# Kernel tuning notes

Measured on AMD Instinct MI355X. Metric: run time of the kernel, lower is better.

## Reference

```python
import jax, jax.numpy as jnp
import numpy as np

NQ, M, ND, N, H, DIM = 32, 32, 200, 160, 768, 128
TEMP = 0.1      # log_softmax temperature
TAU = 0.5       # gumbel-softmax temperature
NEG = -10000.0


def _l2norm(x):
    # F.normalize(p=2, dim=-1) with eps clamp
    n = jnp.maximum(jnp.linalg.norm(x, axis=-1, keepdims=True), 1e-12)
    return x / n


def setup_inputs() -> dict:
    key = jax.random.key(0)
    k1, k2, k3, k4, k5, k6 = jax.random.split(key, 6)
    Q = jax.random.normal(k1, (NQ, M, H), dtype=jnp.float32)
    D = jax.random.normal(k2, (ND, N, H), dtype=jnp.float32)
    q_mask = jax.random.randint(k3, (NQ, M), 0, 2).astype(jnp.float32)
    d_mask = jax.random.randint(k4, (ND, N), 0, 2).astype(jnp.float32)
    # pre-sampled Gumbel(0,1) noise for gumbel_softmax (fixed for determinism)
    u = jax.random.uniform(k5, (NQ, ND, M, N), dtype=jnp.float32,
                           minval=1e-6, maxval=1.0 - 1e-6)
    gumbel_noise = -jnp.log(-jnp.log(u))
    # proj_linear: Linear(768, dim, bias=False)
    W_proj = jax.random.normal(k6, (H, DIM), dtype=jnp.float32) / np.sqrt(H)
    return {"Q": Q, "D": D, "q_mask": q_mask, "d_mask": d_mask,
            "gumbel_noise": gumbel_noise, "W_proj": W_proj}


def reference(Q, D, q_mask, d_mask, gumbel_noise, W_proj):
    # project + L2-normalize token embeddings
    Qp = _l2norm(Q @ W_proj)            # [q, m, dim]
    Dp = _l2norm(D @ W_proj)            # [d, n, dim]

    # pairwise token similarities: [q, d, m, n]
    sim = jnp.einsum('qmh,dnh->qdmn', Qp, Dp)

    dm = d_mask[None, :, None, :]       # [1, d, 1, n]
    sim_masked = sim * dm + (1.0 - dm) * NEG

    logits = jax.nn.log_softmax(sim_masked / TEMP, axis=-1)

    # gumbel_softmax(tau=0.5, hard=True) with straight-through
    y_soft = jax.nn.softmax((logits + gumbel_noise) / TAU, axis=-1)
    idx = jnp.argmax(y_soft, axis=-1)
    y_hard = jax.nn.one_hot(idx, N, dtype=y_soft.dtype)
    y = jax.lax.stop_gradient(y_hard - y_soft) + y_soft

    # select doc token per query token, mask query tokens, sum -> [q, d]
    scores = (y * sim_masked).sum(-1)          # [q, d, m]
    scores = scores * q_mask[:, None, :]
    return scores.sum(-1)                      # [q, d]
```

## Files before the change

### kernel.cpp

```cpp
#include <hip/hip_runtime.h>
#include <math.h>

#define NQ_   32
#define M_    32
#define ND_   200
#define N_    160
#define H_    768
#define DIM_  128
#define DROWS_ (ND_ * N_)
#define QROWS_ (NQ_ * M_)
#define TROWS_ (DROWS_ + QROWS_)

__device__ __forceinline__ void gl_lds16(const float* g, float* l) {
    __builtin_amdgcn_global_load_lds(
        (const __attribute__((address_space(1))) unsigned int*)g,
        (__attribute__((address_space(3))) unsigned int*)l, 16, 0, 0);
}

__global__ __launch_bounds__(128) void proj_kernel(
    const float* __restrict__ Dmat, const float* __restrict__ Qmat,
    const float* __restrict__ W, float* __restrict__ DpT,
    float* __restrict__ QpT)
{
    __shared__ __align__(16) float Xt[2][16][32];
    __shared__ __align__(16) float Ws[2][16][128];
    const int tid  = threadIdx.x;
    const int lane = tid & 63;
    const int wv   = tid >> 6;
    const int rb   = blockIdx.x * 32;
    const int cg   = tid & 15;
    const int rg   = tid >> 4;
    const int xrow = tid >> 2;
    const int xc4  = tid & 3;

    const int rX = rb + xrow;
    const float* xr = (rX < DROWS_) ? (Dmat + (size_t)rX * H_)
                                    : (Qmat + (size_t)(rX - DROWS_) * H_);

    float acc[4][8];
#pragma unroll
    for (int i = 0; i < 4; ++i)
#pragma unroll
        for (int j = 0; j < 8; ++j) acc[i][j] = 0.0f;

#pragma unroll
    for (int t = 0; t < 4; ++t) {
        const int part = wv * 4 + t;
        gl_lds16(W + part * 256 + lane * 4, &Ws[0][0][0] + part * 256);
    }
    float4 xreg = *reinterpret_cast<const float4*>(xr + xc4 * 4);

    for (int c = 0; c < 48; ++c) {
        const int cb = c & 1;
        Xt[cb][xc4*4+0][xrow] = xreg.x;
        Xt[cb][xc4*4+1][xrow] = xreg.y;
        Xt[cb][xc4*4+2][xrow] = xreg.z;
        Xt[cb][xc4*4+3][xrow] = xreg.w;
        __syncthreads();
        if (c < 47) {
            const int kc = (c + 1) * 16;
            const float* wsrc = W + (size_t)kc * DIM_;
            float* wdst = &Ws[cb ^ 1][0][0];
#pragma unroll
            for (int t = 0; t < 4; ++t) {
                const int part = wv * 4 + t;
                gl_lds16(wsrc + part * 256 + lane * 4, wdst + part * 256);
            }
            xreg = *reinterpret_cast<const float4*>(xr + kc + xc4 * 4);
        }
        __builtin_amdgcn_sched_barrier(0);
#pragma unroll
        for (int k = 0; k < 16; ++k) {
            float a[4], b[8];
            *reinterpret_cast<float4*>(&a[0]) = *reinterpret_cast<const float4*>(&Xt[cb][k][rg*4]);
            *reinterpret_cast<float4*>(&b[0]) = *reinterpret_cast<const float4*>(&Ws[cb][k][cg*8]);
            *reinterpret_cast<float4*>(&b[4]) = *reinterpret_cast<const float4*>(&Ws[cb][k][cg*8+4]);
#pragma unroll
            for (int i = 0; i < 4; ++i)
#pragma unroll
                for (int j = 0; j < 8; ++j)
                    acc[i][j] = fmaf(a[i], b[j], acc[i][j]);
        }
    }

    float nrm[4];
#pragma unroll
    for (int i = 0; i < 4; ++i) {
        float ss = 0.0f;
#pragma unroll
        for (int j = 0; j < 8; ++j) ss = __fadd_rn(ss, __fmul_rn(acc[i][j], acc[i][j]));
        ss = __fadd_rn(ss, __shfl_xor(ss, 1));
        ss = __fadd_rn(ss, __shfl_xor(ss, 2));
        ss = __fadd_rn(ss, __shfl_xor(ss, 4));
        ss = __fadd_rn(ss, __shfl_xor(ss, 8));
        nrm[i] = fmaxf(sqrtf(ss), 1e-12f);
    }

    if (rb < DROWS_) {
        const int dd = rb / 160, n0 = rb - dd * 160;
        float* o = DpT + (size_t)dd * (DIM_ * N_) + n0 + rg * 4;
#pragma unroll
        for (int j = 0; j < 8; ++j) {
            float4 v;
            v.x = acc[0][j] / nrm[0];
            v.y = acc[1][j] / nrm[1];
            v.z = acc[2][j] / nrm[2];
            v.w = acc[3][j] / nrm[3];
            *reinterpret_cast<float4*>(o + (size_t)(cg*8 + j) * N_) = v;
        }
    } else {
        const int rq = rb - DROWS_;
        const int qq = rq >> 5;
        float* o = QpT + (size_t)qq * (DIM_ * M_) + rg * 4;
#pragma unroll
        for (int j = 0; j < 8; ++j) {
            float4 v;
            v.x = acc[0][j] / nrm[0];
            v.y = acc[1][j] / nrm[1];
            v.z = acc[2][j] / nrm[2];
            v.w = acc[3][j] / nrm[3];
            *reinterpret_cast<float4*>(o + (size_t)(cg*8 + j) * M_) = v;
        }
    }
}

__global__ __launch_bounds__(128) void score_kernel(
    const float* __restrict__ QpT, const float* __restrict__ DpT,
    const float* __restrict__ qmask, const float* __restrict__ dmask,
    const float* __restrict__ gum, float* __restrict__ out)
{
    __shared__ __align__(16) float Qt[2][8][32];
    __shared__ __align__(16) float Dt[2][8][160];
    __shared__ float red[2];
    const int tid  = threadIdx.x;
    const int lane = tid & 63;
    const int wv   = tid >> 6;
    const int mg   = tid >> 4;
    const int ng   = tid & 15;
    const int q    = blockIdx.x & 31;
    const int d    = blockIdx.x >> 5;

    const float* Qb = QpT + (size_t)q * (DIM_ * M_);
    const float* Db = DpT + (size_t)d * (DIM_ * N_);

    float acc[4][10];
#pragma unroll
    for (int i = 0; i < 4; ++i)
#pragma unroll
        for (int j = 0; j < 10; ++j) acc[i][j] = 0.0f;

    if (wv == 0) {
        gl_lds16(Qb + lane * 4, &Qt[0][0][0]);
        gl_lds16(Db + lane * 4, &Dt[0][0][0]);
        gl_lds16(Db + 256 + lane * 4, &Dt[0][0][0] + 256);
    } else {
        gl_lds16(Db + 512  + lane * 4, &Dt[0][0][0] + 512);
        gl_lds16(Db + 768  + lane * 4, &Dt[0][0][0] + 768);
        gl_lds16(Db + 1024 + lane * 4, &Dt[0][0][0] + 1024);
    }

    for (int c = 0; c < 16; ++c) {
        const int cb = c & 1;
        __syncthreads();
        if (c < 15) {
            const float* qsrc = Qb + (size_t)(c + 1) * 8 * M_;
            const float* dsrc = Db + (size_t)(c + 1) * 8 * N_;
            float* qdst = &Qt[cb ^ 1][0][0];
            float* ddst = &Dt[cb ^ 1][0][0];
            if (wv == 0) {
                gl_lds16(qsrc + lane * 4, qdst);
                gl_lds16(dsrc + lane * 4, ddst);
                gl_lds16(dsrc + 256 + lane * 4, ddst + 256);
            } else {
                gl_lds16(dsrc + 512  + lane * 4, ddst + 512);
                gl_lds16(dsrc + 768  + lane * 4, ddst + 768);
                gl_lds16(dsrc + 1024 + lane * 4, ddst + 1024);
            }
        }
        __builtin_amdgcn_sched_barrier(0);
#pragma unroll
        for (int k = 0; k < 8; ++k) {
            float a[4], b[10];
            *reinterpret_cast<float4*>(&a[0]) = *reinterpret_cast<const float4*>(&Qt[cb][k][mg*4]);
            const float* bp = &Dt[cb][k][ng*10];
#pragma unroll
            for (int j2 = 0; j2 < 5; ++j2)
                *reinterpret_cast<float2*>(&b[j2*2]) = *reinterpret_cast<const float2*>(&bp[j2*2]);
#pragma unroll
            for (int i = 0; i < 4; ++i)
#pragma unroll
                for (int j = 0; j < 10; ++j)
                    acc[i][j] = fmaf(a[i], b[j], acc[i][j]);
        }
    }

    float dmv[10];
    {
        const float* dmp = dmask + (size_t)d * N_ + ng * 10;
#pragma unroll
        for (int j2 = 0; j2 < 5; ++j2)
            *reinterpret_cast<float2*>(&dmv[j2*2]) = *reinterpret_cast<const float2*>(&dmp[j2*2]);
    }

    const float* gq = gum + ((size_t)q * ND_ + d) * ((size_t)M_ * N_);

    float g[2][10];
    {
        const float2* gp = reinterpret_cast<const float2*>(&gq[(size_t)(mg*4) * N_ + ng*10]);
#pragma unroll
        for (int j2 = 0; j2 < 5; ++j2)
            *reinterpret_cast<float2*>(&g[0][j2*2]) = gp[j2];
    }

    float partial = 0.0f;
#pragma unroll
    for (int i = 0; i < 4; ++i) {
        const int m = mg * 4 + i;
        float x[10];
        float mx = -3.402823466e38f;
#pragma unroll
        for (int j = 0; j < 10; ++j) {
            float sm = (dmv[j] != 0.0f) ? acc[i][j] : -10000.0f;
            x[j] = sm / 0.1f;
            mx = fmaxf(mx, x[j]);
        }
        if (i < 3) {
            const float2* gp = reinterpret_cast<const float2*>(&gq[(size_t)(m + 1) * N_ + ng*10]);
#pragma unroll
            for (int j2 = 0; j2 < 5; ++j2)
                *reinterpret_cast<float2*>(&g[(i+1)&1][j2*2]) = gp[j2];
        }
        mx = fmaxf(mx, __shfl_xor(mx, 1));
        mx = fmaxf(mx, __shfl_xor(mx, 2));
        mx = fmaxf(mx, __shfl_xor(mx, 4));
        mx = fmaxf(mx, __shfl_xor(mx, 8));

        float se = 0.0f;
#pragma unroll
        for (int j = 0; j < 10; ++j) se = __fadd_rn(se, expf(x[j] - mx));
        se = __fadd_rn(se, __shfl_xor(se, 1));
        se = __fadd_rn(se, __shfl_xor(se, 2));
        se = __fadd_rn(se, __shfl_xor(se, 4));
        se = __fadd_rn(se, __shfl_xor(se, 8));
        const float lse = logf(se);

        float z[10];
        float mz = -3.402823466e38f;
#pragma unroll
        for (int j = 0; j < 10; ++j) {
            z[j] = ((x[j] - mx - lse) + g[i&1][j]) / 0.5f;
            mz = fmaxf(mz, z[j]);
        }
        mz = fmaxf(mz, __shfl_xor(mz, 1));
        mz = fmaxf(mz, __shfl_xor(mz, 2));
        mz = fmaxf(mz, __shfl_xor(mz, 4));
        mz = fmaxf(mz, __shfl_xor(mz, 8));

        float e2[10];
        float s2 = 0.0f;
#pragma unroll
        for (int j = 0; j < 10; ++j) { e2[j] = expf(z[j] - mz); s2 = __fadd_rn(s2, e2[j]); }
        s2 = __fadd_rn(s2, __shfl_xor(s2, 1));
        s2 = __fadd_rn(s2, __shfl_xor(s2, 2));
        s2 = __fadd_rn(s2, __shfl_xor(s2, 4));
        s2 = __fadd_rn(s2, __shfl_xor(s2, 8));

        float besty = -1.0f; int bestn = 0x7fffffff; float bests = 0.0f;
#pragma unroll
        for (int j = 0; j < 10; ++j) {
            float y = e2[j] / s2;
            if (y > besty) {
                besty = y;
                bestn = ng*10 + j;
                bests = (dmv[j] != 0.0f) ? acc[i][j] : -10000.0f;
            }
        }
#pragma unroll
        for (int dl = 1; dl < 16; dl <<= 1) {
            float oy = __shfl_xor(besty, dl);
            int   on = __shfl_xor(bestn, dl);
            float os = __shfl_xor(bests, dl);
            if (oy > besty || (oy == besty && on < bestn)) {
                besty = oy; bestn = on; bests = os;
            }
        }
        const float qmv = qmask[q * M_ + m];
        if (ng == 0) partial = __fadd_rn(partial, __fmul_rn(bests, qmv));
    }
    partial = __fadd_rn(partial, __shfl_xor(partial, 16));
    partial = __fadd_rn(partial, __shfl_xor(partial, 32));
    if (lane == 0) red[wv] = partial;
    __syncthreads();
    if (tid == 0) out[(size_t)q * ND_ + d] = __fadd_rn(red[0], red[1]);
}

extern "C" void kernel_launch(void* const* d_in, const int* in_sizes, int n_in,
                              void* d_out, int out_size, void* d_ws, size_t ws_size,
                              hipStream_t stream)
{
    const float* Q   = (const float*)d_in[0];
    const float* D   = (const float*)d_in[1];
    const float* qm  = (const float*)d_in[2];
    const float* dm  = (const float*)d_in[3];
    const float* gum = (const float*)d_in[4];
    const float* W   = (const float*)d_in[5];
    float* out = (float*)d_out;

    float* QpT = (float*)d_ws;
    float* DpT = QpT + (size_t)QROWS_ * DIM_;

    proj_kernel<<<dim3(TROWS_ / 32), dim3(128), 0, stream>>>(D, Q, W, DpT, QpT);
    score_kernel<<<dim3(NQ_ * ND_), dim3(128), 0, stream>>>(QpT, DpT, qm, dm, gum, out);
}
```

Baseline: 509.0 us.

## Triple-buffer projection and score loads; single-wave score blocks without barriers

The projection kernel now uses a three-slot ring buffer for W tiles and waits on explicit vmcnt counters before each barrier, so loads run two chunks ahead. The score kernel drops to one 64-thread wave per (q,d) pair, with each thread owning 8 query rows. That wave-local design lets it replace __syncthreads with vmcnt waits on a three-deep LDS pipeline and skip the final shared-memory reduction. Gumbel-noise and qmask loads are issued earlier. The cost is more registers per thread and fewer threads per block, which may lower occupancy and latency hiding, and the hand-tuned waitcnt values must match the number of loads in flight.

Result: slower. 649.3 us (+27.6%).

```diff
diff --git a/kernel.cpp b/kernel.cpp
--- a/kernel.cpp
+++ b/kernel.cpp
@@ -17,13 +17,16 @@
         (__attribute__((address_space(3))) unsigned int*)l, 16, 0, 0);
 }
 
+#define ASM_VMCNT(n) asm volatile("s_waitcnt vmcnt(" #n ")" ::: "memory")
+#define ASM_LGKM0    asm volatile("s_waitcnt lgkmcnt(0)" ::: "memory")
+
 __global__ __launch_bounds__(128) void proj_kernel(
     const float* __restrict__ Dmat, const float* __restrict__ Qmat,
     const float* __restrict__ W, float* __restrict__ DpT,
     float* __restrict__ QpT)
 {
     __shared__ __align__(16) float Xt[2][16][32];
-    __shared__ __align__(16) float Ws[2][16][128];
+    __shared__ __align__(16) float Ws[3][16][128];
     const int tid  = threadIdx.x;
     const int lane = tid & 63;
     const int wv   = tid >> 6;
@@ -34,8 +37,8 @@
     const int xc4  = tid & 3;
 
     const int rX = rb + xrow;
-    const float* xr = (rX < DROWS_) ? (Dmat + (size_t)rX * H_)
-                                    : (Qmat + (size_t)(rX - DROWS_) * H_);
+    const float* xr_ptr = (rX < DROWS_) ? (Dmat + (size_t)rX * H_)
+                                        : (Qmat + (size_t)(rX - DROWS_) * H_);
 
     float acc[4][8];
 #pragma unroll
@@ -48,38 +51,86 @@
         const int part = wv * 4 + t;
         gl_lds16(W + part * 256 + lane * 4, &Ws[0][0][0] + part * 256);
     }
-    float4 xreg = *reinterpret_cast<const float4*>(xr + xc4 * 4);
-
-    for (int c = 0; c < 48; ++c) {
-        const int cb = c & 1;
-        Xt[cb][xc4*4+0][xrow] = xreg.x;
-        Xt[cb][xc4*4+1][xrow] = xreg.y;
-        Xt[cb][xc4*4+2][xrow] = xreg.z;
-        Xt[cb][xc4*4+3][xrow] = xreg.w;
-        __syncthreads();
-        if (c < 47) {
-            const int kc = (c + 1) * 16;
-            const float* wsrc = W + (size_t)kc * DIM_;
-            float* wdst = &Ws[cb ^ 1][0][0];
-#pragma unroll
-            for (int t = 0; t < 4; ++t) {
-                const int part = wv * 4 + t;
-                gl_lds16(wsrc + part * 256 + lane * 4, wdst + part * 256);
-            }
-            xreg = *reinterpret_cast<const float4*>(xr + kc + xc4 * 4);
-        }
-        __builtin_amdgcn_sched_barrier(0);
-#pragma unroll
-        for (int k = 0; k < 16; ++k) {
-            float a[4], b[8];
-            *reinterpret_cast<float4*>(&a[0]) = *reinterpret_cast<const float4*>(&Xt[cb][k][rg*4]);
-            *reinterpret_cast<float4*>(&b[0]) = *reinterpret_cast<const float4*>(&Ws[cb][k][cg*8]);
-            *reinterpret_cast<float4*>(&b[4]) = *reinterpret_cast<const float4*>(&Ws[cb][k][cg*8+4]);
-#pragma unroll
-            for (int i = 0; i < 4; ++i)
-#pragma unroll
-                for (int j = 0; j < 8; ++j)
-                    acc[i][j] = fmaf(a[i], b[j], acc[i][j]);
+    float4 xr0 = *reinterpret_cast<const float4*>(xr_ptr + 0 + xc4 * 4);
+#pragma unroll
+    for (int t = 0; t < 4; ++t) {
+        const int part = wv * 4 + t;
+        gl_lds16(W + 16 * DIM_ + part * 256 + lane * 4, &Ws[1][0][0] + part * 256);
+    }
+    float4 xr1 = *reinterpret_cast<const float4*>(xr_ptr + 16 + xc4 * 4);
+
+    int b0 = 0;
+    for (int c = 0; c < 48; c += 2) {
+        {
+            Xt[0][xc4*4+0][xrow] = xr0.x;
+            Xt[0][xc4*4+1][xrow] = xr0.y;
+            Xt[0][xc4*4+2][xrow] = xr0.z;
+            Xt[0][xc4*4+3][xrow] = xr0.w;
+            ASM_VMCNT(5);
+            ASM_LGKM0;
+            __builtin_amdgcn_s_barrier();
+            if (c + 2 < 48) {
+                const int kc = (c + 2) * 16;
+                const int b2 = (b0 + 2 >= 3) ? b0 - 1 : b0 + 2;
+                float* wdst = &Ws[0][0][0] + b2 * 2048;
+                const float* wsrc = W + (size_t)kc * DIM_;
+#pragma unroll
+                for (int t = 0; t < 4; ++t) {
+                    const int part = wv * 4 + t;
+                    gl_lds16(wsrc + part * 256 + lane * 4, wdst + part * 256);
+                }
+                xr0 = *reinterpret_cast<const float4*>(xr_ptr + kc + xc4 * 4);
+            }
+            __builtin_amdgcn_sched_barrier(0);
+            const float* wb = &Ws[0][0][0] + b0 * 2048;
+#pragma unroll
+            for (int k = 0; k < 16; ++k) {
+                float a[4], b[8];
+                *reinterpret_cast<float4*>(&a[0]) = *reinterpret_cast<const float4*>(&Xt[0][k][rg*4]);
+                *reinterpret_cast<float4*>(&b[0]) = *reinterpret_cast<const float4*>(wb + k*128 + cg*8);
+                *reinterpret_cast<float4*>(&b[4]) = *reinterpret_cast<const float4*>(wb + k*128 + cg*8 + 4);
+#pragma unroll
+                for (int i = 0; i < 4; ++i)
+#pragma unroll
+                    for (int j = 0; j < 8; ++j)
+                        acc[i][j] = fmaf(a[i], b[j], acc[i][j]);
+            }
+        }
+        {
+            const int b1 = (b0 + 1 >= 3) ? b0 - 2 : b0 + 1;
+            Xt[1][xc4*4+0][xrow] = xr1.x;
+            Xt[1][xc4*4+1][xrow] = xr1.y;
+            Xt[1][xc4*4+2][xrow] = xr1.z;
+            Xt[1][xc4*4+3][xrow] = xr1.w;
+            ASM_VMCNT(5);
+            ASM_LGKM0;
+            __builtin_amdgcn_s_barrier();
+            if (c + 3 < 48) {
+                const int kc = (c + 3) * 16;
+                float* wdst = &Ws[0][0][0] + b0 * 2048;
+                const float* wsrc = W + (size_t)kc * DIM_;
+#pragma unroll
+                for (int t = 0; t < 4; ++t) {
+                    const int part = wv * 4 + t;
+                    gl_lds16(wsrc + part * 256 + lane * 4, wdst + part * 256);
+                }
+                xr1 = *reinterpret_cast<const float4*>(xr_ptr + kc + xc4 * 4);
+            }
+            __builtin_amdgcn_sched_barrier(0);
+            const float* wb = &Ws[0][0][0] + b1 * 2048;
+#pragma unroll
+            for (int k = 0; k < 16; ++k) {
+                float a[4], b[8];
+                *reinterpret_cast<float4*>(&a[0]) = *reinterpret_cast<const float4*>(&Xt[1][k][rg*4]);
+                *reinterpret_cast<float4*>(&b[0]) = *reinterpret_cast<const float4*>(wb + k*128 + cg*8);
+                *reinterpret_cast<float4*>(&b[4]) = *reinterpret_cast<const float4*>(wb + k*128 + cg*8 + 4);
+#pragma unroll
+                for (int i = 0; i < 4; ++i)
+#pragma unroll
+                    for (int j = 0; j < 8; ++j)
+                        acc[i][j] = fmaf(a[i], b[j], acc[i][j]);
+            }
+            b0 = (b0 + 2 >= 3) ? b0 - 1 : b0 + 2;
         }
     }
 
@@ -124,76 +175,31 @@
     }
 }
 
-__global__ __launch_bounds__(128) void score_kernel(
+__global__ __launch_bounds__(64) void score_kernel(
     const float* __restrict__ QpT, const float* __restrict__ DpT,
     const float* __restrict__ qmask, const float* __restrict__ dmask,
     const float* __restrict__ gum, float* __restrict__ out)
 {
-    __shared__ __align__(16) float Qt[2][8][32];
-    __shared__ __align__(16) float Dt[2][8][160];
-    __shared__ float red[2];
-    const int tid  = threadIdx.x;
-    const int lane = tid & 63;
-    const int wv   = tid >> 6;
-    const int mg   = tid >> 4;
-    const int ng   = tid & 15;
+    __shared__ __align__(16) float Qt[3][8][32];
+    __shared__ __align__(16) float Dt[3][8][160];
+    const int lane = threadIdx.x;
+    const int mg   = lane >> 4;
+    const int ng   = lane & 15;
     const int q    = blockIdx.x & 31;
     const int d    = blockIdx.x >> 5;
 
     const float* Qb = QpT + (size_t)q * (DIM_ * M_);
     const float* Db = DpT + (size_t)d * (DIM_ * N_);
-
-    float acc[4][10];
-#pragma unroll
-    for (int i = 0; i < 4; ++i)
-#pragma unroll
-        for (int j = 0; j < 10; ++j) acc[i][j] = 0.0f;
-
-    if (wv == 0) {
-        gl_lds16(Qb + lane * 4, &Qt[0][0][0]);
-        gl_lds16(Db + lane * 4, &Dt[0][0][0]);
-        gl_lds16(Db + 256 + lane * 4, &Dt[0][0][0] + 256);
-    } else {
-        gl_lds16(Db + 512  + lane * 4, &Dt[0][0][0] + 512);
-        gl_lds16(Db + 768  + lane * 4, &Dt[0][0][0] + 768);
-        gl_lds16(Db + 1024 + lane * 4, &Dt[0][0][0] + 1024);
-    }
-
-    for (int c = 0; c < 16; ++c) {
-        const int cb = c & 1;
-        __syncthreads();
-        if (c < 15) {
-            const float* qsrc = Qb + (size_t)(c + 1) * 8 * M_;
-            const float* dsrc = Db + (size_t)(c + 1) * 8 * N_;
-            float* qdst = &Qt[cb ^ 1][0][0];
-            float* ddst = &Dt[cb ^ 1][0][0];
-            if (wv == 0) {
-                gl_lds16(qsrc + lane * 4, qdst);
-                gl_lds16(dsrc + lane * 4, ddst);
-                gl_lds16(dsrc + 256 + lane * 4, ddst + 256);
-            } else {
-                gl_lds16(dsrc + 512  + lane * 4, ddst + 512);
-                gl_lds16(dsrc + 768  + lane * 4, ddst + 768);
-                gl_lds16(dsrc + 1024 + lane * 4, ddst + 1024);
-            }
-        }
-        __builtin_amdgcn_sched_barrier(0);
-#pragma unroll
-        for (int k = 0; k < 8; ++k) {
-            float a[4], b[10];
-            *reinterpret_cast<float4*>(&a[0]) = *reinterpret_cast<const float4*>(&Qt[cb][k][mg*4]);
-            const float* bp = &Dt[cb][k][ng*10];
-#pragma unroll
-            for (int j2 = 0; j2 < 5; ++j2)
-                *reinterpret_cast<float2*>(&b[j2*2]) = *reinterpret_cast<const float2*>(&bp[j2*2]);
-#pragma unroll
-            for (int i = 0; i < 4; ++i)
-#pragma unroll
-                for (int j = 0; j < 10; ++j)
-                    acc[i][j] = fmaf(a[i], b[j], acc[i][j]);
-        }
-    }
-
+    const float* gq = gum + ((size_t)q * ND_ + d) * ((size_t)M_ * N_);
+
+    float g[2][10];
+#pragma unroll
+    for (int r = 0; r < 2; ++r) {
+        const float2* gp = reinterpret_cast<const float2*>(&gq[(size_t)(mg*8 + r) * N_ + ng*10]);
+#pragma unroll
+        for (int j2 = 0; j2 < 5; ++j2)
+            *reinterpret_cast<float2*>(&g[r][j2*2]) = gp[j2];
+    }
     float dmv[10];
     {
         const float* dmp = dmask + (size_t)d * N_ + ng * 10;
@@ -201,21 +207,64 @@
         for (int j2 = 0; j2 < 5; ++j2)
             *reinterpret_cast<float2*>(&dmv[j2*2]) = *reinterpret_cast<const float2*>(&dmp[j2*2]);
     }
-
-    const float* gq = gum + ((size_t)q * ND_ + d) * ((size_t)M_ * N_);
-
-    float g[2][10];
-    {
-        const float2* gp = reinterpret_cast<const float2*>(&gq[(size_t)(mg*4) * N_ + ng*10]);
-#pragma unroll
-        for (int j2 = 0; j2 < 5; ++j2)
-            *reinterpret_cast<float2*>(&g[0][j2*2]) = gp[j2];
-    }
+    float qmv[8];
+#pragma unroll
+    for (int i = 0; i < 8; ++i) qmv[i] = qmask[q * M_ + mg*8 + i];
+
+    float acc[8][10];
+#pragma unroll
+    for (int i = 0; i < 8; ++i)
+#pragma unroll
+        for (int j = 0; j < 10; ++j) acc[i][j] = 0.0f;
+
+#define ISSUE_CHUNK(c_)                                                     \
+    do {                                                                    \
+        const int b_ = (c_) % 3;                                            \
+        const float* qs_ = Qb + (size_t)(c_) * 8 * M_;                      \
+        const float* ds_ = Db + (size_t)(c_) * 8 * N_;                      \
+        float* qd_ = &Qt[b_][0][0];                                         \
+        float* dd_ = &Dt[b_][0][0];                                         \
+        gl_lds16(qs_ + lane * 4, qd_);                                      \
+        gl_lds16(ds_ + 0   + lane * 4, dd_ + 0);                            \
+        gl_lds16(ds_ + 256 + lane * 4, dd_ + 256);                          \
+        gl_lds16(ds_ + 512 + lane * 4, dd_ + 512);                          \
+        gl_lds16(ds_ + 768 + lane * 4, dd_ + 768);                          \
+        gl_lds16(ds_ + 1024 + lane * 4, dd_ + 1024);                        \
+    } while (0)
+
+    ISSUE_CHUNK(0);
+    ISSUE_CHUNK(1);
+
+    for (int c = 0; c < 16; ++c) {
+        if (c < 15) { ASM_VMCNT(6); }
+        else        { ASM_VMCNT(0); }
+        if (c < 14) ISSUE_CHUNK(c + 2);
+        __builtin_amdgcn_sched_barrier(0);
+        const int cb = c % 3;
+        const float* qtb = &Qt[cb][0][0];
+        const float* dtb = &Dt[cb][0][0];
+#pragma unroll
+        for (int k = 0; k < 8; ++k) {
+            float a[8], b[10];
+            *reinterpret_cast<float4*>(&a[0]) = *reinterpret_cast<const float4*>(qtb + k*32 + mg*8);
+            *reinterpret_cast<float4*>(&a[4]) = *reinterpret_cast<const float4*>(qtb + k*32 + mg*8 + 4);
+            const float* bp = dtb + k*160 + ng*10;
+#pragma unroll
+            for (int j2 = 0; j2 < 5; ++j2)
+                *reinterpret_cast<float2*>(&b[j2*2]) = *reinterpret_cast<const float2*>(&bp[j2*2]);
+#pragma unroll
+            for (int i = 0; i < 8; ++i)
+#pragma unroll
+                for (int j = 0; j < 10; ++j)
+                    acc[i][j] = fmaf(a[i], b[j], acc[i][j]);
+        }
+    }
+#undef ISSUE_CHUNK
 
     float partial = 0.0f;
 #pragma unroll
-    for (int i = 0; i < 4; ++i) {
-        const int m = mg * 4 + i;
+    for (int i = 0; i < 8; ++i) {
+        const int m = mg*8 + i;
         float x[10];
         float mx = -3.402823466e38f;
 #pragma unroll
@@ -223,12 +272,6 @@
             float sm = (dmv[j] != 0.0f) ? acc[i][j] : -10000.0f;
             x[j] = sm / 0.1f;
             mx = fmaxf(mx, x[j]);
-        }
-        if (i < 3) {
-            const float2* gp = reinterpret_cast<const float2*>(&gq[(size_t)(m + 1) * N_ + ng*10]);
-#pragma unroll
-            for (int j2 = 0; j2 < 5; ++j2)
-                *reinterpret_cast<float2*>(&g[(i+1)&1][j2*2]) = gp[j2];
         }
         mx = fmaxf(mx, __shfl_xor(mx, 1));
         mx = fmaxf(mx, __shfl_xor(mx, 2));
@@ -248,8 +291,14 @@
         float mz = -3.402823466e38f;
 #pragma unroll
         for (int j = 0; j < 10; ++j) {
-            z[j] = ((x[j] - mx - lse) + g[i&1][j]) / 0.5f;
+            z[j] = ((x[j] - mx - lse) + g[i & 1][j]) / 0.5f;
             mz = fmaxf(mz, z[j]);
+        }
+        if (i < 6) {
+            const float2* gp = reinterpret_cast<const float2*>(&gq[(size_t)(m + 2) * N_ + ng*10]);
+#pragma unroll
+            for (int j2 = 0; j2 < 5; ++j2)
+                *reinterpret_cast<float2*>(&g[i & 1][j2*2]) = gp[j2];
         }
         mz = fmaxf(mz, __shfl_xor(mz, 1));
         mz = fmaxf(mz, __shfl_xor(mz, 2));
@@ -284,14 +333,11 @@
                 besty = oy; bestn = on; bests = os;
             }
         }
-        const float qmv = qmask[q * M_ + m];
-        if (ng == 0) partial = __fadd_rn(partial, __fmul_rn(bests, qmv));
+        if (ng == 0) partial = __fadd_rn(partial, __fmul_rn(bests, qmv[i]));
     }
     partial = __fadd_rn(partial, __shfl_xor(partial, 16));
     partial = __fadd_rn(partial, __shfl_xor(partial, 32));
-    if (lane == 0) red[wv] = partial;
-    __syncthreads();
-    if (tid == 0) out[(size_t)q * ND_ + d] = __fadd_rn(red[0], red[1]);
+    if (lane == 0) out[(size_t)q * ND_ + d] = partial;
 }
 
 extern "C" void kernel_launch(void* const* d_in, const int* in_sizes, int n_in,
@@ -310,5 +356,5 @@
     float* DpT = QpT + (size_t)QROWS_ * DIM_;
 
     proj_kernel<<<dim3(TROWS_ / 32), dim3(128), 0, stream>>>(D, Q, W, DpT, QpT);
-    score_kernel<<<dim3(NQ_ * ND_), dim3(128), 0, stream>>>(QpT, DpT, qm, dm, gum, out);
+    score_kernel<<<dim3(NQ_ * ND_), dim3(64), 0, stream>>>(QpT, DpT, qm, dm, gum, out);
 }
```
